# Kernel optimization log

Hardware: AMD Instinct MI355X
Metric: run time of the kernel (lower is better)

The kernel has to match this reference:

```python
import jax, jax.numpy as jnp
import numpy as np

N, E, F, H, L, G, EMB, C = 50000, 600000, 128, 128, 4, 64, 64, 10
BN_EPS = 1e-5


def setup_inputs() -> dict:
    key = jax.random.key(0)
    k = lambda i: jax.random.fold_in(key, i)
    s = 0.05  # weight scale
    return {
        "x": jax.random.normal(k(0), (N, F), jnp.float32),
        "edge_index": jax.random.randint(k(1), (2, E), 0, N, jnp.int64),
        "batch": jnp.sort(jax.random.randint(k(2), (N,), 0, G, jnp.int64)),
        "emb": jax.random.normal(k(3), (G, EMB), jnp.float32),
        "eps": jnp.zeros((L,), jnp.float32),
        "W1": jax.random.normal(k(4), (L, F, H), jnp.float32) * s,
        "b1": jnp.zeros((L, H), jnp.float32),
        "W2": jax.random.normal(k(5), (L, H, H), jnp.float32) * s,
        "b2": jnp.zeros((L, H), jnp.float32),
        "gamma": jnp.ones((L, H), jnp.float32),
        "beta": jnp.zeros((L, H), jnp.float32),
        "lin1_w": jax.random.normal(k(6), (L * H + EMB, 2 * H), jnp.float32) * s,
        "lin1_b": jnp.zeros((2 * H,), jnp.float32),
        "lin2_w": jax.random.normal(k(7), (2 * H, H), jnp.float32) * s,
        "lin2_b": jnp.zeros((H,), jnp.float32),
        "lin4_w": jax.random.normal(k(8), (H, C), jnp.float32) * s,
        "lin4_b": jnp.zeros((C,), jnp.float32),
    }


def _gin_mlp(h, W1, b1, W2, b2, gamma, beta):
    # Linear -> ReLU -> Linear -> ReLU -> BatchNorm1d (batch stats)
    h = jax.nn.relu(h @ W1 + b1)
    h = jax.nn.relu(h @ W2 + b2)
    mean = jnp.mean(h, axis=0)
    var = jnp.var(h, axis=0)
    return (h - mean) * jax.lax.rsqrt(var + BN_EPS) * gamma + beta


def reference(x, edge_index, batch, emb, eps, W1, b1, W2, b2, gamma, beta,
              lin1_w, lin1_b, lin2_w, lin2_b, lin4_w, lin4_b):
    src, dst = edge_index[0], edge_index[1]
    xs = []
    for l in range(L):
        # GIN: MLP((1+eps)*x_i + sum_{j->i} x_j)  via gather + scatter-add
        agg = jax.ops.segment_sum(x[src], dst, num_segments=N)  # [N,H]
        x = _gin_mlp((1.0 + eps[l]) * x + agg,
                     W1[l], b1[l], W2[l], b2[l], gamma[l], beta[l])
        xs.append(x)
    h = jnp.concatenate(xs, axis=1)  # [N, L*H]
    # global mean pool per graph
    sums = jax.ops.segment_sum(h, batch, num_segments=G)  # [G, L*H]
    cnt = jax.ops.segment_sum(jnp.ones((N,), h.dtype), batch, num_segments=G)
    pooled = sums / jnp.maximum(cnt, 1.0)[:, None]
    z = jnp.concatenate([pooled, emb.reshape(G, -1)], axis=1)
    z = jax.nn.relu(z @ lin1_w + lin1_b)  # .relu() twice is idempotent
    # dropout p=0.5 skipped (eval mode); lin3 unused in original forward
    z = jax.nn.relu(z @ lin2_w + lin2_b)
    z = z @ lin4_w + lin4_b
    return jax.nn.log_softmax(z, axis=1)
```

## Files before the change

### kernel.cpp

```cpp
#include <hip/hip_runtime.h>
#include <cstdint>
#include <cstddef>

#define N_NODES 50000
#define N_EDGES 600000
#define NLAYER  4
#define NGRAPH  64
#define SCAN_NB 196
#define MROWS   64
#define NBLK_MLP ((N_NODES + MROWS - 1) / MROWS)
#define CVTX_NB ((N_NODES * 32 + 255) / 256)
#define CVTW_NB ((NLAYER * 128 * 128 * 2) / 256)
#define DEG_NB  ((N_EDGES + 255) / 256)

typedef unsigned int   u32;
typedef unsigned short u16;
typedef unsigned char  u8;
typedef float f32x4  __attribute__((ext_vector_type(4)));
typedef short bf16x8 __attribute__((ext_vector_type(8)));

__device__ __forceinline__ u16 f2bf(float f) {
    u32 x = __float_as_uint(f);
    u32 r = x + 0x7fffu + ((x >> 16) & 1u);
    return (u16)(r >> 16);
}
__device__ __forceinline__ u32 pack2(float a, float b) {
    return (u32)f2bf(a) | ((u32)f2bf(b) << 16);
}

__device__ __forceinline__ float fp8b0(u32 u) { return __builtin_amdgcn_cvt_f32_fp8(u, 0); }
__device__ __forceinline__ float fp8b1(u32 u) { return __builtin_amdgcn_cvt_f32_fp8(u, 1); }
__device__ __forceinline__ u32 pk_fp8(float a, float b) {
    return (u32)__builtin_amdgcn_cvt_pk_fp8_f32(a, b, 0, false);
}

__global__ __launch_bounds__(256) void setup_all(
    const float4* __restrict__ x, u32* __restrict__ xf8,
    const float* __restrict__ W1, const float* __restrict__ W2,
    short* __restrict__ W1t, short* __restrict__ W2t,
    const int* __restrict__ dst, int* __restrict__ deg,
    int* __restrict__ rank) {
    int b = blockIdx.x, tid = threadIdx.x;
    if (b < CVTX_NB) {
        int i = b * 256 + tid;
        if (i < N_NODES * 32) {
            float4 v = x[i];
            u32 r = pk_fp8(v.x, v.y);
            r = (u32)__builtin_amdgcn_cvt_pk_fp8_f32(v.z, v.w, (int)r, true);
            xf8[i] = r;
        }
    } else if (b < CVTX_NB + CVTW_NB) {
        int i = (b - CVTX_NB) * 256 + tid;
        int z = i >> 16, r = i & 65535;
        int l = r >> 14, n = (r >> 7) & 127, k = r & 127;
        const float* W = z ? W2 : W1;
        short* Wt      = z ? W2t : W1t;
        Wt[((size_t)l * 128 + n) * 128 + k] = (short)f2bf(W[((size_t)l * 128 + k) * 128 + n]);
    } else {
        int e = (b - CVTX_NB - CVTW_NB) * 256 + tid;
        if (e < N_EDGES) rank[e] = atomicAdd(&deg[dst[e]], 1);
    }
}

__global__ __launch_bounds__(256) void scan_l1(const int* __restrict__ deg,
                                               int* __restrict__ bscan,
                                               int* __restrict__ bsum) {
    __shared__ int sd[256];
    int tid = threadIdx.x;
    int i = blockIdx.x * 256 + tid;
    int v = (i < N_NODES) ? deg[i] : 0;
    sd[tid] = v; __syncthreads();
#pragma unroll
    for (int off = 1; off < 256; off <<= 1) {
        int t = (tid >= off) ? sd[tid - off] : 0;
        __syncthreads();
        sd[tid] += t; __syncthreads();
    }
    if (i < N_NODES) bscan[i] = sd[tid];
    if (tid == 255) bsum[blockIdx.x] = sd[255];
}

__global__ __launch_bounds__(256) void scan_l3(const int* __restrict__ bscan,
                                               const int* __restrict__ bsum,
                                               int* __restrict__ rowp) {
    __shared__ int sd[256];
    __shared__ int sboff;
    int tid = threadIdx.x;
    int v = (tid < SCAN_NB) ? bsum[tid] : 0;
    sd[tid] = v; __syncthreads();
#pragma unroll
    for (int off = 1; off < 256; off <<= 1) {
        int t = (tid >= off) ? sd[tid - off] : 0;
        __syncthreads();
        sd[tid] += t; __syncthreads();
    }
    if (tid == (int)blockIdx.x) sboff = sd[tid] - v;
    __syncthreads();
    int i = blockIdx.x * 256 + tid;
    if (i == 0) rowp[0] = 0;
    if (i < N_NODES) rowp[i + 1] = bscan[i] + sboff;
}

__global__ __launch_bounds__(256) void fill_csr(
    const int* __restrict__ src, const int* __restrict__ dst,
    const int* __restrict__ rowp, const int* __restrict__ rank,
    int* __restrict__ col) {
    int e = blockIdx.x * 256 + threadIdx.x;
    if (e < N_EDGES) col[rowp[dst[e]] + rank[e]] = src[e];
}

__global__ __launch_bounds__(256) void agg_kernel(
    const u16* __restrict__ xin,
    const float* __restrict__ sums_prev,
    const float* __restrict__ gamma, const float* __restrict__ beta,
    int layer, const float* __restrict__ eps_all,
    const int* __restrict__ rowp, const int* __restrict__ col,
    u32* __restrict__ agg) {
    __shared__ float cA[128], cD[128];
    int tid = threadIdx.x;
    if (tid < 128) {
        float a = 1.f, d = 0.f;
        if (sums_prev) {
            float s1 = sums_prev[tid], s2 = sums_prev[128 + tid];
            float mean = s1 * (1.0f / N_NODES);
            float var  = s2 * (1.0f / N_NODES) - mean * mean;
            a = rsqrtf(var + 1e-5f) * gamma[(layer - 1) * 128 + tid];
            d = beta[(layer - 1) * 128 + tid] - mean * a;
        }
        cA[tid] = a; cD[tid] = d;
    }
    __syncthreads();
    int node = blockIdx.x * 4 + (tid >> 6);
    int lane = tid & 63;
    if (node >= N_NODES) return;
    float a0 = cA[2 * lane], a1 = cA[2 * lane + 1];
    float d0 = cD[2 * lane], d1 = cD[2 * lane + 1];
    float ep = 1.0f + eps_all[layer];
    u32 v = xin[(size_t)node * 64 + lane];
    int k0 = rowp[node], k1 = rowp[node + 1];
    float s0 = 0.f, s1 = 0.f;
    int k = k0;
    int cc[8];
    if (k < k1) {
#pragma unroll
        for (int t = 0; t < 8; t++) cc[t] = col[min(k + t, k1 - 1)];
    }
    while (k < k1) {
        int idx[8];
#pragma unroll
        for (int t = 0; t < 8; t++) idx[t] = cc[t];
        int kn = k + 8;
        if (kn < k1) {
#pragma unroll
            for (int t = 0; t < 8; t++) cc[t] = col[min(kn + t, k1 - 1)];
        }
#pragma unroll
        for (int t = 0; t < 8; t++) {
            u32 u = xin[(size_t)idx[t] * 64 + lane];
            float w = (k + t < k1) ? 1.f : 0.f;
            s0 += w * fp8b0(u); s1 += w * fp8b1(u);
        }
        k = kn;
    }
    float deg = (float)(k1 - k0);
    float r0 = ep * (a0 * fp8b0(v) + d0) + a0 * s0 + deg * d0;
    float r1 = ep * (a1 * fp8b1(v) + d1) + a1 * s1 + deg * d1;
    agg[(size_t)node * 64 + lane] = pack2(r0, r1);
}

#define H1_STR 136
__global__ __launch_bounds__(256) void mlp_fused(
    const short* __restrict__ A,
    const short* __restrict__ W1t, const float* __restrict__ b1,
    const short* __restrict__ W2t, const float* __restrict__ b2,
    u8* __restrict__ H2, const int* __restrict__ batch,
    float* __restrict__ sums, float* __restrict__ gsum, int M) {
    __shared__ alignas(16) short h1s[MROWS * H1_STR];
    __shared__ float scr[3 * 4 * 128];
    __shared__ int sh_ga, sh_gb, sh_split;
    int tid  = threadIdx.x;
    int wave = tid >> 6, lane = tid & 63;
    int ln15 = lane & 15, quad = lane >> 4;
    int m0blk = blockIdx.x * MROWS;
    int row0 = m0blk + wave * 16;
    const bf16x8 zz = {0, 0, 0, 0, 0, 0, 0, 0};

    if (tid == 0) {
        int rlo = m0blk, rhi = min(m0blk + MROWS - 1, M - 1);
        int ga = batch[rlo], gb = batch[rhi];
        int split = m0blk + MROWS;
        if (ga != gb) {
            int lo = rlo, hi = rhi;
            while (lo + 1 < hi) { int mid = (lo + hi) >> 1; if (batch[mid] == ga) lo = mid; else hi = mid; }
            split = hi;
        }
        sh_ga = ga; sh_gb = gb; sh_split = split;
    }

    bf16x8 a[4];
    {
        int row = row0 + ln15;
        const short* rp = A + (size_t)row * 128 + quad * 8;
        bool ok = row < M;
#pragma unroll
        for (int s = 0; s < 4; s++)
            a[s] = ok ? *(const bf16x8*)(rp + s * 32) : zz;
    }
#pragma unroll
    for (int ct = 0; ct < 8; ct++) {
        const short* wp = W1t + (size_t)(ct * 16 + ln15) * 128 + quad * 8;
        bf16x8 b[4];
#pragma unroll
        for (int s = 0; s < 4; s++) b[s] = *(const bf16x8*)(wp + s * 32);
        float bias = b1[ct * 16 + ln15];
        f32x4 acc = {0.f, 0.f, 0.f, 0.f};
#pragma unroll
        for (int s = 0; s < 4; s++)
            acc = __builtin_amdgcn_mfma_f32_16x16x32_bf16(a[s], b[s], acc, 0, 0, 0);
#pragma unroll
        for (int i = 0; i < 4; i++) {
            float v = fmaxf(acc[i] + bias, 0.f);
            int lr = wave * 16 + quad * 4 + i;
            h1s[lr * H1_STR + ct * 16 + ln15] = (short)f2bf(v);
        }
    }
    __syncthreads();
    bf16x8 c[4];
#pragma unroll
    for (int s = 0; s < 4; s++)
        c[s] = *(const bf16x8*)&h1s[(wave * 16 + ln15) * H1_STR + quad * 8 + s * 32];

    int gsplit = sh_split;
    float sAcc[8], qAcc[8], pAcc[8];
#pragma unroll
    for (int ct = 0; ct < 8; ct++) { sAcc[ct] = 0.f; qAcc[ct] = 0.f; pAcc[ct] = 0.f; }
#pragma unroll
    for (int ct = 0; ct < 8; ct++) {
        const short* wp = W2t + (size_t)(ct * 16 + ln15) * 128 + quad * 8;
        bf16x8 b[4];
#pragma unroll
        for (int s = 0; s < 4; s++) b[s] = *(const bf16x8*)(wp + s * 32);
        float bias = b2[ct * 16 + ln15];
        f32x4 acc = {0.f, 0.f, 0.f, 0.f};
#pragma unroll
        for (int s = 0; s < 4; s++)
            acc = __builtin_amdgcn_mfma_f32_16x16x32_bf16(c[s], b[s], acc, 0, 0, 0);
        int colx = ct * 16 + ln15;
#pragma unroll
        for (int i = 0; i < 4; i++) {
            int row = row0 + quad * 4 + i;
            float v = fmaxf(acc[i] + bias, 0.f);
            if (row < M) H2[(size_t)row * 128 + colx] = (u8)(pk_fp8(v, v) & 0xffu);
            float vm = (row < M) ? v : 0.f;
            sAcc[ct] += vm; qAcc[ct] += vm * vm;
            if (row < gsplit) pAcc[ct] += vm;
        }
    }
#pragma unroll
    for (int ct = 0; ct < 8; ct++) {
        sAcc[ct] += __shfl_xor(sAcc[ct], 16); sAcc[ct] += __shfl_xor(sAcc[ct], 32);
        qAcc[ct] += __shfl_xor(qAcc[ct], 16); qAcc[ct] += __shfl_xor(qAcc[ct], 32);
        pAcc[ct] += __shfl_xor(pAcc[ct], 16); pAcc[ct] += __shfl_xor(pAcc[ct], 32);
    }
    if (quad == 0) {
#pragma unroll
        for (int ct = 0; ct < 8; ct++) {
            int colx = ct * 16 + ln15;
            scr[(0 * 4 + wave) * 128 + colx] = sAcc[ct];
            scr[(1 * 4 + wave) * 128 + colx] = qAcc[ct];
            scr[(2 * 4 + wave) * 128 + colx] = pAcc[ct];
        }
    }
    __syncthreads();
    if (tid < 128) {
        float ss = 0.f, qq = 0.f, pa = 0.f;
#pragma unroll
        for (int w = 0; w < 4; w++) {
            ss += scr[(0 * 4 + w) * 128 + tid];
            qq += scr[(1 * 4 + w) * 128 + tid];
            pa += scr[(2 * 4 + w) * 128 + tid];
        }
        atomicAdd(&sums[tid], ss);
        atomicAdd(&sums[128 + tid], qq);
        int ga = sh_ga, gb = sh_gb;
        atomicAdd(&gsum[ga * 128 + tid], pa);
        if (gb != ga) atomicAdd(&gsum[gb * 128 + tid], ss - pa);
    }
}

__global__ __launch_bounds__(256) void head_kernel(
    const float* __restrict__ gsum, const float* __restrict__ sumsL,
    const float* __restrict__ gamma, const float* __restrict__ beta,
    const int* __restrict__ batch, const float* __restrict__ emb,
    const float* __restrict__ l1w, const float* __restrict__ l1b,
    const float* __restrict__ l2w, const float* __restrict__ l2b,
    const float* __restrict__ l4w, const float* __restrict__ l4b,
    float* __restrict__ out) {
    __shared__ float z[576];
    __shared__ float z1[256];
    __shared__ float z2h[2][128];
    __shared__ float z2[128];
    __shared__ float zr[128][10];
    __shared__ float inv_cnt;
    int g = blockIdx.x;
    int tid = threadIdx.x;
    if (tid == 0) {
        int lo = 0, hi = N_NODES;
        while (lo < hi) { int m = (lo + hi) >> 1; if (batch[m] < g) lo = m + 1; else hi = m; }
        int s = lo;
        lo = 0; hi = N_NODES;
        while (lo < hi) { int m = (lo + hi) >> 1; if (batch[m] < g + 1) lo = m + 1; else hi = m; }
        inv_cnt = 1.0f / fmaxf((float)(lo - s), 1.0f);
    }
    __syncthreads();
    for (int j = tid; j < 512; j += 256) {
        int l = j >> 7, c = j & 127;
        float s1 = sumsL[l * 256 + c], s2 = sumsL[l * 256 + 128 + c];
        float mean = s1 * (1.0f / N_NODES);
        float var  = s2 * (1.0f / N_NODES) - mean * mean;
        float a = rsqrtf(var + 1e-5f) * gamma[l * 128 + c];
        float d = beta[l * 128 + c] - mean * a;
        z[j] = a * gsum[(size_t)l * NGRAPH * 128 + g * 128 + c] * inv_cnt + d;
    }
    if (tid < 64) z[512 + tid] = emb[g * 64 + tid];
    __syncthreads();
    {
        float acc = l1b[tid];
        for (int j0 = 0; j0 < 576; j0 += 16) {
            float lw[16];
#pragma unroll
            for (int t = 0; t < 16; t++) lw[t] = l1w[(j0 + t) * 256 + tid];
#pragma unroll
            for (int t = 0; t < 16; t++) acc += z[j0 + t] * lw[t];
        }
        z1[tid] = fmaxf(acc, 0.f);
    }
    __syncthreads();
    {
        int c2 = tid & 127, half = tid >> 7;
        float acc = 0.f;
        int jb = half * 128;
        for (int j0 = 0; j0 < 128; j0 += 8) {
            float lw[8];
#pragma unroll
            for (int t = 0; t < 8; t++) lw[t] = l2w[(jb + j0 + t) * 128 + c2];
#pragma unroll
            for (int t = 0; t < 8; t++) acc += z1[jb + j0 + t] * lw[t];
        }
        z2h[half][c2] = acc;
    }
    __syncthreads();
    if (tid < 128) z2[tid] = fmaxf(z2h[0][tid] + z2h[1][tid] + l2b[tid], 0.f);
    __syncthreads();
    if (tid < 128) {
        float zv = z2[tid];
        const float* wr = l4w + tid * 10;
#pragma unroll
        for (int c = 0; c < 10; c++) zr[tid][c] = zv * wr[c];
    }
    __syncthreads();
    for (int s = 64; s >= 1; s >>= 1) {
        if (tid < s) {
#pragma unroll
            for (int c = 0; c < 10; c++) zr[tid][c] += zr[tid + s][c];
        }
        __syncthreads();
    }
    if (tid == 0) {
        float z3s[10];
#pragma unroll
        for (int c = 0; c < 10; c++) z3s[c] = zr[0][c] + l4b[c];
        float m = z3s[0];
        for (int i = 1; i < 10; i++) m = fmaxf(m, z3s[i]);
        float se = 0.f;
        for (int i = 0; i < 10; i++) se += expf(z3s[i] - m);
        float lse = m + logf(se);
        for (int i = 0; i < 10; i++) out[g * 10 + i] = z3s[i] - lse;
    }
}

extern "C" void kernel_launch(void* const* d_in, const int* in_sizes, int n_in,
                              void* d_out, int out_size, void* d_ws, size_t ws_size,
                              hipStream_t stream) {
    (void)in_sizes; (void)n_in; (void)out_size; (void)ws_size;
    const float* x0   = (const float*)d_in[0];
    const int* ei     = (const int*)d_in[1];
    const int* src    = ei;
    const int* dst    = ei + N_EDGES;
    const int* batch  = (const int*)d_in[2];
    const float* emb  = (const float*)d_in[3];
    const float* eps  = (const float*)d_in[4];
    const float* W1   = (const float*)d_in[5];
    const float* b1   = (const float*)d_in[6];
    const float* W2   = (const float*)d_in[7];
    const float* b2   = (const float*)d_in[8];
    const float* gamma= (const float*)d_in[9];
    const float* beta = (const float*)d_in[10];
    const float* l1w  = (const float*)d_in[11];
    const float* l1b  = (const float*)d_in[12];
    const float* l2w  = (const float*)d_in[13];
    const float* l2b  = (const float*)d_in[14];
    const float* l4w  = (const float*)d_in[15];
    const float* l4b  = (const float*)d_in[16];

    char* ws = (char*)d_ws;
    size_t off = 0;
    auto alloc = [&](size_t bytes) -> char* {
        char* p = ws + off; off += (bytes + 255) & ~(size_t)255; return p;
    };
    int* deg    = (int*)alloc(N_NODES * 4);
    float* sumsL = (float*)alloc(NLAYER * 256 * 4);
    float* gsumL = (float*)alloc((size_t)NLAYER * NGRAPH * 128 * 4);
    size_t zero_len = (char*)gsumL - (char*)deg + (size_t)NLAYER * NGRAPH * 128 * 4;
    int* rowp   = (int*)alloc((N_NODES + 1) * 4);
    int* bscan  = (int*)alloc(N_NODES * 4);
    int* bsum   = (int*)alloc(SCAN_NB * 4);
    int* col    = (int*)alloc(N_EDGES * 4);
    int* rank   = (int*)alloc(N_EDGES * 4);
    u8* xf8     = (u8*)alloc((size_t)N_NODES * 128);
    u8* h2a     = (u8*)alloc((size_t)N_NODES * 128);
    u8* h2b     = (u8*)alloc((size_t)N_NODES * 128);
    u32* agg    = (u32*)alloc((size_t)N_NODES * 64 * 4);
    short* W1t  = (short*)alloc((size_t)NLAYER * 128 * 128 * 2);
    short* W2t  = (short*)alloc((size_t)NLAYER * 128 * 128 * 2);

    hipMemsetAsync(deg, 0, zero_len, stream);

    setup_all<<<CVTX_NB + CVTW_NB + DEG_NB, 256, 0, stream>>>(
        (const float4*)x0, (u32*)xf8, W1, W2, W1t, W2t, dst, deg, rank);
    scan_l1<<<SCAN_NB, 256, 0, stream>>>(deg, bscan, bsum);
    scan_l3<<<SCAN_NB, 256, 0, stream>>>(bscan, bsum, rowp);
    fill_csr<<<(N_EDGES + 255) / 256, 256, 0, stream>>>(src, dst, rowp, rank, col);

    const u8* xin = xf8;
    for (int l = 0; l < NLAYER; ++l) {
        u8* h2 = (l & 1) ? h2b : h2a;
        const float* sums_prev = (l == 0) ? nullptr : (sumsL + (l - 1) * 256);
        agg_kernel<<<(N_NODES + 3) / 4, 256, 0, stream>>>(
            (const u16*)xin, sums_prev, gamma, beta, l, eps, rowp, col, agg);
        mlp_fused<<<NBLK_MLP, 256, 0, stream>>>(
            (const short*)agg, W1t + (size_t)l * 16384, b1 + l * 128,
            W2t + (size_t)l * 16384, b2 + l * 128, h2, batch,
            sumsL + l * 256, gsumL + (size_t)l * NGRAPH * 128, N_NODES);
        xin = h2;
    }
    head_kernel<<<NGRAPH, 256, 0, stream>>>(gsumL, sumsL, gamma, beta, batch, emb,
                                            l1w, l1b, l2w, l2b, l4w, l4b,
                                            (float*)d_out);
}
```

Measured before the change: 458.7 us.

## Stage MLP weights in shared memory and build CSR with a cursor array

New measurement: 489.0 us. 6.6% more time.

```diff
diff --git a/kernel.cpp b/kernel.cpp
--- a/kernel.cpp
+++ b/kernel.cpp
@@ -38,8 +38,7 @@
     const float4* __restrict__ x, u32* __restrict__ xf8,
     const float* __restrict__ W1, const float* __restrict__ W2,
     short* __restrict__ W1t, short* __restrict__ W2t,
-    const int* __restrict__ dst, int* __restrict__ deg,
-    int* __restrict__ rank) {
+    const int* __restrict__ dst, int* __restrict__ deg) {
     int b = blockIdx.x, tid = threadIdx.x;
     if (b < CVTX_NB) {
         int i = b * 256 + tid;
@@ -58,7 +57,7 @@
         Wt[((size_t)l * 128 + n) * 128 + k] = (short)f2bf(W[((size_t)l * 128 + k) * 128 + n]);
     } else {
         int e = (b - CVTX_NB - CVTW_NB) * 256 + tid;
-        if (e < N_EDGES) rank[e] = atomicAdd(&deg[dst[e]], 1);
+        if (e < N_EDGES) atomicAdd(&deg[dst[e]], 1);
     }
 }
 
@@ -101,12 +100,15 @@
     if (i < N_NODES) rowp[i + 1] = bscan[i] + sboff;
 }
 
-__global__ __launch_bounds__(256) void fill_csr(
-    const int* __restrict__ src, const int* __restrict__ dst,
-    const int* __restrict__ rowp, const int* __restrict__ rank,
-    int* __restrict__ col) {
+__global__ void fill_csr(const int* __restrict__ src, const int* __restrict__ dst,
+                         const int* __restrict__ rowp, int* __restrict__ cursor,
+                         int* __restrict__ col) {
     int e = blockIdx.x * 256 + threadIdx.x;
-    if (e < N_EDGES) col[rowp[dst[e]] + rank[e]] = src[e];
+    if (e < N_EDGES) {
+        int d = dst[e];
+        int pos = atomicAdd(&cursor[d], 1);
+        col[rowp[d] + pos] = src[e];
+    }
 }
 
 __global__ __launch_bounds__(256) void agg_kernel(
@@ -169,14 +171,15 @@
 }
 
 #define H1_STR 136
+#define WSTR   132
 __global__ __launch_bounds__(256) void mlp_fused(
     const short* __restrict__ A,
     const short* __restrict__ W1t, const float* __restrict__ b1,
     const short* __restrict__ W2t, const float* __restrict__ b2,
     u8* __restrict__ H2, const int* __restrict__ batch,
     float* __restrict__ sums, float* __restrict__ gsum, int M) {
+    __shared__ alignas(16) short wbuf[128 * WSTR];
     __shared__ alignas(16) short h1s[MROWS * H1_STR];
-    __shared__ float scr[3 * 4 * 128];
     __shared__ int sh_ga, sh_gb, sh_split;
     int tid  = threadIdx.x;
     int wave = tid >> 6, lane = tid & 63;
@@ -206,9 +209,24 @@
         for (int s = 0; s < 4; s++)
             a[s] = ok ? *(const bf16x8*)(rp + s * 32) : zz;
     }
+    bf16x8 wr1[8], wr2[8];
+#pragma unroll
+    for (int i = 0; i < 8; i++)
+        wr1[i] = *(const bf16x8*)(W1t + (size_t)(i * 256 + tid) * 8);
+#pragma unroll
+    for (int i = 0; i < 8; i++)
+        wr2[i] = *(const bf16x8*)(W2t + (size_t)(i * 256 + tid) * 8);
+
+#pragma unroll
+    for (int i = 0; i < 8; i++) {
+        int idx = i * 256 + tid;
+        *(bf16x8*)&wbuf[(idx >> 4) * WSTR + (idx & 15) * 8] = wr1[i];
+    }
+    __syncthreads();
+
 #pragma unroll
     for (int ct = 0; ct < 8; ct++) {
-        const short* wp = W1t + (size_t)(ct * 16 + ln15) * 128 + quad * 8;
+        const short* wp = &wbuf[(ct * 16 + ln15) * WSTR + quad * 8];
         bf16x8 b[4];
 #pragma unroll
         for (int s = 0; s < 4; s++) b[s] = *(const bf16x8*)(wp + s * 32);
@@ -225,10 +243,17 @@
         }
     }
     __syncthreads();
+
+#pragma unroll
+    for (int i = 0; i < 8; i++) {
+        int idx = i * 256 + tid;
+        *(bf16x8*)&wbuf[(idx >> 4) * WSTR + (idx & 15) * 8] = wr2[i];
+    }
     bf16x8 c[4];
 #pragma unroll
     for (int s = 0; s < 4; s++)
         c[s] = *(const bf16x8*)&h1s[(wave * 16 + ln15) * H1_STR + quad * 8 + s * 32];
+    __syncthreads();
 
     int gsplit = sh_split;
     float sAcc[8], qAcc[8], pAcc[8];
@@ -236,7 +261,7 @@
     for (int ct = 0; ct < 8; ct++) { sAcc[ct] = 0.f; qAcc[ct] = 0.f; pAcc[ct] = 0.f; }
 #pragma unroll
     for (int ct = 0; ct < 8; ct++) {
-        const short* wp = W2t + (size_t)(ct * 16 + ln15) * 128 + quad * 8;
+        const short* wp = &wbuf[(ct * 16 + ln15) * WSTR + quad * 8];
         bf16x8 b[4];
 #pragma unroll
         for (int s = 0; s < 4; s++) b[s] = *(const bf16x8*)(wp + s * 32);
@@ -262,6 +287,8 @@
         qAcc[ct] += __shfl_xor(qAcc[ct], 16); qAcc[ct] += __shfl_xor(qAcc[ct], 32);
         pAcc[ct] += __shfl_xor(pAcc[ct], 16); pAcc[ct] += __shfl_xor(pAcc[ct], 32);
     }
+    __syncthreads();
+    float* scr = (float*)wbuf;
     if (quad == 0) {
 #pragma unroll
         for (int ct = 0; ct < 8; ct++) {
@@ -409,6 +436,7 @@
         char* p = ws + off; off += (bytes + 255) & ~(size_t)255; return p;
     };
     int* deg    = (int*)alloc(N_NODES * 4);
+    int* cursor = (int*)alloc(N_NODES * 4);
     float* sumsL = (float*)alloc(NLAYER * 256 * 4);
     float* gsumL = (float*)alloc((size_t)NLAYER * NGRAPH * 128 * 4);
     size_t zero_len = (char*)gsumL - (char*)deg + (size_t)NLAYER * NGRAPH * 128 * 4;
@@ -416,7 +444,6 @@
     int* bscan  = (int*)alloc(N_NODES * 4);
     int* bsum   = (int*)alloc(SCAN_NB * 4);
     int* col    = (int*)alloc(N_EDGES * 4);
-    int* rank   = (int*)alloc(N_EDGES * 4);
     u8* xf8     = (u8*)alloc((size_t)N_NODES * 128);
     u8* h2a     = (u8*)alloc((size_t)N_NODES * 128);
     u8* h2b     = (u8*)alloc((size_t)N_NODES * 128);
@@ -427,10 +454,10 @@
     hipMemsetAsync(deg, 0, zero_len, stream);
 
     setup_all<<<CVTX_NB + CVTW_NB + DEG_NB, 256, 0, stream>>>(
-        (const float4*)x0, (u32*)xf8, W1, W2, W1t, W2t, dst, deg, rank);
+        (const float4*)x0, (u32*)xf8, W1, W2, W1t, W2t, dst, deg);
     scan_l1<<<SCAN_NB, 256, 0, stream>>>(deg, bscan, bsum);
     scan_l3<<<SCAN_NB, 256, 0, stream>>>(bscan, bsum, rowp);
-    fill_csr<<<(N_EDGES + 255) / 256, 256, 0, stream>>>(src, dst, rowp, rank, col);
+    fill_csr<<<(N_EDGES + 255) / 256, 256, 0, stream>>>(src, dst, rowp, cursor, col);
 
     const u8* xin = xf8;
     for (int l = 0; l < NLAYER; ++l) {
```
